# Optimization experiments

Hardware: AMD Instinct MI355X
Metric: run time of the kernel (lower is better)

The kernel has to match this reference:

```python
import jax, jax.numpy as jnp
import numpy as np

N = 50000      # nodes
E = 800000     # edges
GENE = 64      # gene_dim
HID = 128      # hidden_dim
NCLS = 10      # num_classes
EPS = 1e-5


def setup_inputs() -> dict:
    key = jax.random.key(0)
    ks = jax.random.split(key, 4)
    inp = {
        "x": jax.random.normal(ks[0], (N, GENE), jnp.float32),
        "edge_index": jax.random.randint(ks[1], (2, E), 0, N),
    }
    # PNA-style conv: concat([x, 4 aggregators x 3 scalers]) -> 13*d_in features
    dims = [(GENE, HID), (HID, 2 * HID), (2 * HID, HID), (HID, HID // 2)]
    for i, (din, dout) in enumerate(dims, 1):
        k = jax.random.fold_in(key, i)
        inp[f"W{i}"] = jax.random.normal(k, (13 * din, dout), jnp.float32) / float(np.sqrt(13 * din))
        inp[f"b{i}"] = jnp.zeros((dout,), jnp.float32)
        inp[f"gamma{i}"] = jnp.ones((dout,), jnp.float32)
        inp[f"beta{i}"] = jnp.zeros((dout,), jnp.float32)
    inp["Wc"] = jax.random.normal(ks[2], (HID // 2, NCLS), jnp.float32) / float(np.sqrt(HID // 2))
    inp["bc"] = jnp.zeros((NCLS,), jnp.float32)
    return inp


def _pna(x, src, dst, deg, log_deg, delta, W, b):
    # gather source features along edges: [E, d]
    msg = x[src]
    cnt = jnp.maximum(deg, 1.0)[:, None]
    s = jax.ops.segment_sum(msg, dst, num_segments=N)
    mean = s / cnt
    mean_sq = jax.ops.segment_sum(msg * msg, dst, num_segments=N) / cnt
    std = jnp.sqrt(jnp.maximum(mean_sq - mean * mean, 0.0) + EPS)
    has = (deg > 0)[:, None]
    mn = jnp.where(has, jax.ops.segment_min(msg, dst, num_segments=N), 0.0)
    mx = jnp.where(has, jax.ops.segment_max(msg, dst, num_segments=N), 0.0)
    aggs = jnp.concatenate([mean, mn, mx, std], axis=-1)  # [N, 4d]
    amp = (log_deg / delta)[:, None]                       # amplification scaler
    att = jnp.where(log_deg > 0, delta / jnp.maximum(log_deg, 1e-6), 1.0)[:, None]
    feat = jnp.concatenate([x, aggs, aggs * amp, aggs * att], axis=-1)  # [N, 13d]
    return feat @ W + b


def _bn(h, gamma, beta):
    m = h.mean(axis=0)
    v = h.var(axis=0)
    return (h - m) / jnp.sqrt(v + EPS) * gamma + beta


def reference(x, edge_index, W1, b1, gamma1, beta1, W2, b2, gamma2, beta2,
              W3, b3, gamma3, beta3, W4, b4, gamma4, beta4, Wc, bc):
    src, dst = edge_index[0], edge_index[1]
    deg = jax.ops.segment_sum(jnp.ones((E,), jnp.float32), dst, num_segments=N)
    log_deg = jnp.log1p(deg)
    delta = log_deg.mean()
    h = _pna(x, src, dst, deg, log_deg, delta, W1, b1)
    h = _bn(jax.nn.relu(h), gamma1, beta1)
    h = _pna(h, src, dst, deg, log_deg, delta, W2, b2)
    h = _bn(jax.nn.relu(h), gamma2, beta2)
    h = _pna(h, src, dst, deg, log_deg, delta, W3, b3)
    h = _bn(jax.nn.relu(h), gamma3, beta3)
    h = _pna(h, src, dst, deg, log_deg, delta, W4, b4)
    h = _bn(jax.nn.relu(h), gamma4, beta4)
    return h @ Wc + bc
```

## Files before the change

kernel.cpp:

```cpp
#include <hip/hip_runtime.h>
#include <hip/hip_bf16.h>

#define NN 50000
#define NE 800000
#define EPSV 1e-5f
#define NB 49

typedef _Float16 h8 __attribute__((ext_vector_type(8)));
typedef float    f4 __attribute__((ext_vector_type(4)));

#define AS1 __attribute__((address_space(1)))
#define AS3 __attribute__((address_space(3)))

__device__ __forceinline__ void gload_lds16(const _Float16* g, _Float16* l){
  __builtin_amdgcn_global_load_lds((const AS1 void*)g, (AS3 void*)l, 16, 0, 0);
}


__global__ void k_deg(const int* __restrict__ dst, int* __restrict__ deg){
  int e = blockIdx.x*blockDim.x + threadIdx.x;
  if(e < NE) atomicAdd(&deg[dst[e]], 1);
}

__global__ void k_logdeg(const int* __restrict__ deg, float* __restrict__ logdeg,
                         float* __restrict__ dsum){
  int i = blockIdx.x*blockDim.x + threadIdx.x;
  float v = 0.f;
  if(i < NN){ v = log1pf((float)deg[i]); logdeg[i] = v; }
  __shared__ float sh[256];
  sh[threadIdx.x] = v; __syncthreads();
  for(int off=128; off>0; off>>=1){
    if(threadIdx.x < off) sh[threadIdx.x] += sh[threadIdx.x+off];
    __syncthreads();
  }
  if(threadIdx.x == 0) atomicAdd(dsum, sh[0]);
}

__global__ void k_scalers(const float* __restrict__ logdeg, const float* __restrict__ dsum,
                          float* __restrict__ amp, float* __restrict__ att){
  int i = blockIdx.x*blockDim.x + threadIdx.x;
  if(i >= NN) return;
  float delta = dsum[0] / (float)NN;
  float ld = logdeg[i];
  amp[i] = ld / delta;
  att[i] = (ld > 0.f) ? (delta / fmaxf(ld, 1e-6f)) : 1.f;
}

__global__ void k_scan1(const int* __restrict__ deg, int* __restrict__ rowptr,
                        int* __restrict__ bsum){
  __shared__ int buf[1024];
  int tid = threadIdx.x;
  int i = blockIdx.x*1024 + tid;
  int v = (i < NN) ? deg[i] : 0;
  buf[tid] = v; __syncthreads();
  for(int off=1; off<1024; off<<=1){
    int t = (tid >= off) ? buf[tid-off] : 0;
    __syncthreads();
    buf[tid] += t;
    __syncthreads();
  }
  if(i < NN) rowptr[i] = buf[tid] - v;
  if(tid == 1023) bsum[blockIdx.x] = buf[1023];
}

__global__ void k_scan2(int* __restrict__ bsum){
  if(threadIdx.x == 0){
    int s = 0;
    for(int b = 0; b < NB; b++){ int t = bsum[b]; bsum[b] = s; s += t; }
    bsum[NB] = s;
  }
}

__global__ void k_scan3(int* __restrict__ rowptr, int* __restrict__ cursor,
                        const int* __restrict__ bsum){
  int i = blockIdx.x*256 + threadIdx.x;
  if(i < NN){
    int v = rowptr[i] + bsum[i >> 10];
    rowptr[i] = v; cursor[i] = v;
  }
  if(i == NN) rowptr[NN] = bsum[NB];
}

__global__ void k_fill(const int* __restrict__ src, const int* __restrict__ dst,
                       int* __restrict__ cursor, int* __restrict__ colidx){
  int e = blockIdx.x*blockDim.x + threadIdx.x;
  if(e < NE){
    int pos = atomicAdd(&cursor[dst[e]], 1);
    colidx[pos] = src[e];
  }
}

__global__ void k_cvtx(const float* __restrict__ x, _Float16* __restrict__ act){
  int i = blockIdx.x*256 + threadIdx.x;
  if(i < NN*64) act[i] = (_Float16)x[i];
}

__global__ void k_coef_id(float* __restrict__ cs, float* __restrict__ csh,
                          _Float16* __restrict__ cs16, _Float16* __restrict__ csh16){
  int c = threadIdx.x;
  cs[c] = 1.f; csh[c] = 0.f;
  cs16[c] = (_Float16)1.f; csh16[c] = (_Float16)0.f;
}

__global__ void k_bn_coef(const float* __restrict__ colsum, const float* __restrict__ colss,
                          const float* __restrict__ gamma, const float* __restrict__ beta,
                          int dout, float* __restrict__ cs, float* __restrict__ csh,
                          _Float16* __restrict__ cs16, _Float16* __restrict__ csh16){
  int c = threadIdx.x;
  if(c >= dout) return;
  float mean = colsum[c] / (float)NN;
  float var  = colss[c] / (float)NN - mean*mean;
  float inv  = rsqrtf(fmaxf(var, 0.f) + EPSV);
  float a = inv * gamma[c];
  float b = beta[c] - mean * a;
  cs[c] = a; csh[c] = b;
  cs16[c] = (_Float16)a; csh16[c] = (_Float16)b;
}


template<int D>
__global__ __launch_bounds__(256) void k_agg8(
    const _Float16* __restrict__ act,
    const int* __restrict__ rowptr, const int* __restrict__ colidx,
    const float* __restrict__ cs, const float* __restrict__ csh,
    _Float16* __restrict__ aggs, size_t aggN)
{
  constexpr int LPN = D >> 3;
  constexpr int NPW = 64 / LPN;
  int wv = threadIdx.x >> 6, lane = threadIdx.x & 63;
  int n = blockIdx.x*(NPW*4) + wv*NPW + (lane / LPN);
  int c = (lane % LPN) * 8;
  if(n >= NN) return;
  int beg = rowptr[n], end = rowptr[n+1];
  const _Float16* hp = act + c;

  float s[8], q[8], mn[8], mx[8];
  #pragma unroll
  for(int j = 0; j < 8; j++){ s[j]=0.f; q[j]=0.f; mn[j]=INFINITY; mx[j]=-INFINITY; }

#define ACC8(v) { _Pragma("unroll") for(int j=0;j<8;j++){ float a=(float)(v)[j]; \
    s[j]+=a; q[j]+=a*a; mn[j]=fminf(mn[j],a); mx[j]=fmaxf(mx[j],a); } }

  int e = beg;
  for(; e+8 <= end; e+=8){
    int i0=colidx[e],   i1=colidx[e+1], i2=colidx[e+2], i3=colidx[e+3];
    int i4=colidx[e+4], i5=colidx[e+5], i6=colidx[e+6], i7=colidx[e+7];
    h8 v0 = *(const h8*)(hp + (size_t)i0*D);
    h8 v1 = *(const h8*)(hp + (size_t)i1*D);
    h8 v2 = *(const h8*)(hp + (size_t)i2*D);
    h8 v3 = *(const h8*)(hp + (size_t)i3*D);
    h8 v4 = *(const h8*)(hp + (size_t)i4*D);
    h8 v5 = *(const h8*)(hp + (size_t)i5*D);
    h8 v6 = *(const h8*)(hp + (size_t)i6*D);
    h8 v7 = *(const h8*)(hp + (size_t)i7*D);
    ACC8(v0) ACC8(v1) ACC8(v2) ACC8(v3) ACC8(v4) ACC8(v5) ACC8(v6) ACC8(v7)
  }
  for(; e+4 <= end; e+=4){
    int i0=colidx[e], i1=colidx[e+1], i2=colidx[e+2], i3=colidx[e+3];
    h8 v0 = *(const h8*)(hp + (size_t)i0*D);
    h8 v1 = *(const h8*)(hp + (size_t)i1*D);
    h8 v2 = *(const h8*)(hp + (size_t)i2*D);
    h8 v3 = *(const h8*)(hp + (size_t)i3*D);
    ACC8(v0) ACC8(v1) ACC8(v2) ACC8(v3)
  }
  for(; e < end; e++){
    h8 v = *(const h8*)(hp + (size_t)colidx[e]*D);
    ACC8(v)
  }
#undef ACC8

  float cnt = (end>beg) ? (float)(end-beg) : 1.f;
  h8 vm, vn, vx, vs;
  #pragma unroll
  for(int j = 0; j < 8; j++){
    float a = cs[c+j], b = csh[c+j];
    float mean_r = s[j]/cnt;
    float var_r  = fmaxf(q[j]/cnt - mean_r*mean_r, 0.f);
    float meanp = a*mean_r + b;
    float mnp = (a >= 0.f) ? a*mn[j]+b : a*mx[j]+b;
    float mxp = (a >= 0.f) ? a*mx[j]+b : a*mn[j]+b;
    float sdp = sqrtf(a*a*var_r + EPSV);
    if(end <= beg){ meanp = 0.f; mnp = 0.f; mxp = 0.f; sdp = sqrtf(EPSV); }
    vm[j] = (_Float16)meanp; vn[j] = (_Float16)mnp;
    vx[j] = (_Float16)mxp;   vs[j] = (_Float16)sdp;
  }

  _Float16* dst = aggs + (size_t)(c>>6)*aggN + (size_t)n*256 + (c & 63);
  *(h8*)(dst)       = vm;
  *(h8*)(dst + 64)  = vn;
  *(h8*)(dst + 128) = vx;
  *(h8*)(dst + 192) = vs;
}


struct PackJob { const float* W; _Float16* dst; int d, o, j0, start; };
struct PackArgs { PackJob job[9]; int total; };

__global__ void k_pack_all(PackArgs a){
  int idx = blockIdx.x*256 + threadIdx.x;
  if(idx >= a.total) return;
  int ji = 0;
  while(ji < 8 && idx >= a.job[ji+1].start) ji++;
  PackJob J = a.job[ji];
  int rel = idx - J.start;
  int j    = rel & 7;
  int lane = (rel >> 3) & 63;
  int rem  = rel >> 9;
  int ntiles = J.o >> 4;
  int kb = rem / ntiles;
  int nt = rem - kb*ntiles;
  int k = kb*32 + (lane>>4)*8 + j;
  int n = nt*16 + (lane&15);
  int srcrow;
  if(k < 64)       srcrow = J.j0 + k;
  else if(k < 320){ int t=k-64;  srcrow = (1+(t>>6))*J.d + J.j0 + (t&63); }
  else if(k < 576){ int t=k-320; srcrow = (5+(t>>6))*J.d + J.j0 + (t&63); }
  else            { int t=k-576; srcrow = (9+(t>>6))*J.d + J.j0 + (t&63); }
  J.dst[rel] = (_Float16)J.W[(size_t)srcrow*J.o + n];
}


template<int NCH>
__global__ __launch_bounds__(256) void k_mfma_fused(
    const _Float16* __restrict__ actIn,
    const _Float16* __restrict__ aggs,
    const float* __restrict__ amp, const float* __restrict__ att,
    const _Float16* __restrict__ cs16, const _Float16* __restrict__ csh16,
    const _Float16* __restrict__ Wp, int o,
    const float* __restrict__ bias,
    _Float16* __restrict__ out,
    float* __restrict__ colsum, float* __restrict__ colss,
    size_t aggN)
{
  constexpr int D = NCH * 64;
  constexpr int NPH = NCH * 9;
  __shared__ _Float16 Bsm[3][12*512];
  __shared__ float redS[64], redQ[64];
  int tid  = threadIdx.x;
  int wv   = tid >> 6;
  int lane = tid & 63;
  int mi   = lane & 15;
  int q    = lane >> 4;

  int T  = gridDim.x * gridDim.y;
  int n_ = blockIdx.y * gridDim.x + blockIdx.x;
  int qq = T >> 3, rr = T & 7, xc = n_ & 7, nl = n_ >> 3;
  int m_ = (xc < rr ? xc*(qq+1) : rr*(qq+1) + (xc-rr)*qq) + nl;
  int bx = m_ % gridDim.x;
  int by = m_ / gridDim.x;

  int m0   = by * 128 + wv * 32;
  int c0   = bx * 64;
  int ntiles = o >> 4;
  int nt0  = bx * 4;

  if(tid < 64){ redS[tid] = 0.f; redQ[tid] = 0.f; }

  int mrow[2];
  mrow[0] = min(m0 + mi,      NN-1);
  mrow[1] = min(m0 + 16 + mi, NN-1);
  _Float16 am16[2] = { (_Float16)amp[mrow[0]], (_Float16)amp[mrow[1]] };
  _Float16 at16[2] = { (_Float16)att[mrow[0]], (_Float16)att[mrow[1]] };
  const _Float16* hAb[2];
  const _Float16* agb[2];
  hAb[0] = actIn + (size_t)mrow[0]*D + q*8;
  hAb[1] = actIn + (size_t)mrow[1]*D + q*8;
  agb[0] = aggs + (size_t)mrow[0]*256 + q*8;
  agb[1] = aggs + (size_t)mrow[1]*256 + q*8;

  f4 acc[2][4] = {};

  auto stageX = [&](_Float16* buf, int c){
    const _Float16* Wpc = Wp + (size_t)c*832*o;
    #pragma unroll
    for(int s = 0; s < 2; s++){
      int ti = wv*2 + s;
      int kb = ti >> 2, nn = ti & 3;
      gload_lds16(Wpc + (((size_t)kb*ntiles + nt0 + nn)*64 + lane)*8,
                  buf + ti*512);
    }
  };
  auto stageP = [&](_Float16* buf, int c, int idx){
    const _Float16* Wpc = Wp + (size_t)c*832*o;
    #pragma unroll
    for(int s = 0; s < 3; s++){
      int ti = wv*3 + s;
      int kj = ti >> 2, nn = ti & 3;
      int kb = (kj == 0 ? 2 : (kj == 1 ? 10 : 18)) + idx;
      gload_lds16(Wpc + (((size_t)kb*ntiles + nt0 + nn)*64 + lane)*8,
                  buf + ti*512);
    }
  };
  auto stagePh = [&](int p2){
    int c2 = p2 / 9, s2 = p2 % 9;
    _Float16* buf = &Bsm[p2 % 3][0];
    if(s2 == 0) stageX(buf, c2);
    else        stageP(buf, c2, s2 - 1);
  };

  h8 pA[2][4]; h8 pS[2][2]; h8 pH[2][2];
  auto loadA = [&](int ph2, int bank){
    if(ph2 >= NPH) return;
    int c = ph2 / 9, sub = ph2 % 9;
    if(sub == 0){
      #pragma unroll
      for(int kb = 0; kb < 2; kb++){
        pS[bank][kb] = *(const h8*)(cs16  + c*64 + kb*32 + q*8);
        pH[bank][kb] = *(const h8*)(csh16 + c*64 + kb*32 + q*8);
        #pragma unroll
        for(int t = 0; t < 2; t++)
          pA[bank][kb*2+t] = *(const h8*)(hAb[t] + c*64 + kb*32);
      }
    } else {
      int idx = sub - 1;
      #pragma unroll
      for(int t = 0; t < 2; t++)
        pA[bank][t] = *(const h8*)(agb[t] + (size_t)c*aggN + idx*32);
    }
  };

  stagePh(0);
  __builtin_amdgcn_sched_barrier(0);
  stagePh(1);
  __builtin_amdgcn_sched_barrier(0);
  loadA(0, 0);
  loadA(1, 1);
  __builtin_amdgcn_sched_barrier(0);
  asm volatile("s_waitcnt vmcnt(13)\n\ts_barrier" ::: "memory");

  #pragma unroll
  for(int ph = 0; ph < NPH; ph++){
    const int sub = ph % 9;
    const int bank = ph & 1;
    _Float16* cur = &Bsm[ph % 3][0];

    h8 cA[4]; h8 cS[2]; h8 cH[2];
    cA[0] = pA[bank][0]; cA[1] = pA[bank][1];
    if(sub == 0){
      cA[2] = pA[bank][2]; cA[3] = pA[bank][3];
      cS[0] = pS[bank][0]; cS[1] = pS[bank][1];
      cH[0] = pH[bank][0]; cH[1] = pH[bank][1];
    }

    if(ph + 2 < NPH) stagePh(ph + 2);
    __builtin_amdgcn_sched_barrier(0);

    loadA(ph + 2, bank);

    __builtin_amdgcn_s_setprio(1);
    if(sub == 0){
      #pragma unroll
      for(int kb = 0; kb < 2; kb++)
        #pragma unroll
        for(int t = 0; t < 2; t++){
          h8 ax = cA[kb*2+t]*cS[kb] + cH[kb];
          #pragma unroll
          for(int nn = 0; nn < 4; nn++)
            acc[t][nn] = __builtin_amdgcn_mfma_f32_16x16x32_f16(
                ax, *(const h8*)(cur + (kb*4+nn)*512 + lane*8), acc[t][nn], 0,0,0);
        }
    } else {
      #pragma unroll
      for(int t = 0; t < 2; t++){
        h8 apl = cA[t];
        h8 aam = apl * am16[t];
        h8 aat = apl * at16[t];
        #pragma unroll
        for(int nn = 0; nn < 4; nn++){
          acc[t][nn] = __builtin_amdgcn_mfma_f32_16x16x32_f16(
              apl, *(const h8*)(cur + (0*4+nn)*512 + lane*8), acc[t][nn], 0,0,0);
          acc[t][nn] = __builtin_amdgcn_mfma_f32_16x16x32_f16(
              aam, *(const h8*)(cur + (4+nn)*512 + lane*8), acc[t][nn], 0,0,0);
          acc[t][nn] = __builtin_amdgcn_mfma_f32_16x16x32_f16(
              aat, *(const h8*)(cur + (8+nn)*512 + lane*8), acc[t][nn], 0,0,0);
        }
      }
    }
    __builtin_amdgcn_s_setprio(0);

    if(ph + 1 < NPH){
      const bool x1   = ((ph + 1) % 9) == 0;
      const bool has2 = (ph + 2) < NPH;
      const bool x2   = has2 && (((ph + 2) % 9) == 0);
      const int K = (x1 ? 8 : 2) + (has2 ? ((x2 ? 2 : 3) + (x2 ? 8 : 2)) : 0);
      if(K == 13)      asm volatile("s_waitcnt vmcnt(13)\n\ts_barrier" ::: "memory");
      else if(K == 12) asm volatile("s_waitcnt vmcnt(12)\n\ts_barrier" ::: "memory");
      else if(K == 7)  asm volatile("s_waitcnt vmcnt(7)\n\ts_barrier" ::: "memory");
      else             asm volatile("s_waitcnt vmcnt(2)\n\ts_barrier" ::: "memory");
    }
  }

  __syncthreads();

  #pragma unroll
  for(int nn = 0; nn < 4; nn++){
    int n = c0 + nn*16 + mi;
    float bv = bias[n];
    float ps = 0.f, pq = 0.f;
    #pragma unroll
    for(int t = 0; t < 2; t++){
      #pragma unroll
      for(int r = 0; r < 4; r++){
        int m = m0 + t*16 + q*4 + r;
        if(m < NN){
          float v = fmaxf(bv + acc[t][nn][r], 0.f);
          out[(size_t)m*o + n] = (_Float16)v;
          ps += v; pq += v*v;
        }
      }
    }
    ps += __shfl_xor(ps, 16); pq += __shfl_xor(pq, 16);
    ps += __shfl_xor(ps, 32); pq += __shfl_xor(pq, 32);
    if(q == 0){
      atomicAdd(&redS[nn*16 + mi], ps);
      atomicAdd(&redQ[nn*16 + mi], pq);
    }
  }
  __syncthreads();
  if(tid < 64){
    atomicAdd(&colsum[c0 + tid], redS[tid]);
    atomicAdd(&colss[c0 + tid],  redQ[tid]);
  }
}


__global__ __launch_bounds__(256) void k_cls(const _Float16* __restrict__ h,
    const float* __restrict__ cs, const float* __restrict__ csh,
    const float* __restrict__ Wc, const float* __restrict__ bc,
    float* __restrict__ out){
  __shared__ float w[640];
  __shared__ float bb[16];
  __shared__ float sca[64], shb[64];
  int tid = threadIdx.x;
  for(int i = tid; i < 640; i += 256) w[i] = Wc[i];
  if(tid < 10) bb[tid] = bc[tid];
  if(tid < 64){ sca[tid] = cs[tid]; shb[tid] = csh[tid]; }
  __syncthreads();
  int idx = blockIdx.x*256 + tid;
  int n = idx >> 4;
  int c = idx & 15;
  if(n < NN && c < 10){
    float acc = bb[c];
    const _Float16* hp = h + (size_t)n*64;
    #pragma unroll
    for(int k = 0; k < 64; k++)
      acc += ((float)hp[k]*sca[k] + shb[k]) * w[k*10 + c];
    out[(size_t)n*10 + c] = acc;
  }
}


extern "C" void kernel_launch(void* const* d_in, const int* in_sizes, int n_in,
                              void* d_out, int out_size, void* d_ws, size_t ws_size,
                              hipStream_t stream){
  const float* x = (const float*)d_in[0];
  const int* edge = (const int*)d_in[1];
  const int* esrc = edge;
  const int* edst = edge + NE;
  const float* W[4]  = {(const float*)d_in[2],  (const float*)d_in[6],
                        (const float*)d_in[10], (const float*)d_in[14]};
  const float* bb[4] = {(const float*)d_in[3],  (const float*)d_in[7],
                        (const float*)d_in[11], (const float*)d_in[15]};
  const float* gm[4] = {(const float*)d_in[4],  (const float*)d_in[8],
                        (const float*)d_in[12], (const float*)d_in[16]};
  const float* bt[4] = {(const float*)d_in[5],  (const float*)d_in[9],
                        (const float*)d_in[13], (const float*)d_in[17]};
  const float* Wc = (const float*)d_in[18];
  const float* bc = (const float*)d_in[19];
  (void)in_sizes; (void)n_in; (void)out_size; (void)ws_size;

  char* p = (char*)d_ws;
  auto alloc = [&](size_t bytes)->char*{
    char* r = p; p += (bytes + 255) & ~(size_t)255; return r;
  };
  _Float16* act0 = (_Float16*)alloc((size_t)NN*256*2);
  _Float16* act1 = (_Float16*)alloc((size_t)NN*256*2);
  _Float16* aggs = (_Float16*)alloc((size_t)4*NN*256*2);
  int*   deg    = (int*)  alloc((size_t)NN*4);
  float* logdeg = (float*)alloc((size_t)NN*4);
  float* amp    = (float*)alloc((size_t)NN*4);
  float* att    = (float*)alloc((size_t)NN*4);
  int*   rowptr = (int*)  alloc((size_t)(NN+1)*4);
  int*   cursor = (int*)  alloc((size_t)NN*4);
  int*   colidx = (int*)  alloc((size_t)NE*4);
  int*   bsum   = (int*)  alloc((size_t)(NB+1)*4);
  float* colsumL= (float*)alloc(4*256*4);
  float* colssL = (float*)alloc(4*256*4);
  float* dsum   = (float*)alloc(256);
  float*    csA  = (float*)   alloc(256*4);
  float*    cshA = (float*)   alloc(256*4);
  float*    csB  = (float*)   alloc(256*4);
  float*    cshB = (float*)   alloc(256*4);
  _Float16* cs16A  = (_Float16*)alloc(256*2);
  _Float16* csh16A = (_Float16*)alloc(256*2);
  _Float16* cs16B  = (_Float16*)alloc(256*2);
  _Float16* csh16B = (_Float16*)alloc(256*2);

  const int din[4]  = {64, 128, 256, 128};
  const int dto[4]  = {128, 256, 128, 64};
  const size_t aggN = (size_t)NN*256;
  _Float16* WpL[4];
  PackArgs pa; int pj = 0, poff = 0;
  for(int l = 0; l < 4; l++){
    int nch = din[l]/64;
    WpL[l] = (_Float16*)alloc((size_t)nch*832*dto[l]*2);
    for(int c = 0; c < nch; c++){
      pa.job[pj] = { W[l], WpL[l] + (size_t)c*832*dto[l], din[l], dto[l], c*64, poff };
      poff += 832*dto[l]; pj++;
    }
  }
  pa.total = poff;

  hipMemsetAsync(deg, 0, (size_t)NN*4, stream);
  hipMemsetAsync(dsum, 0, 4, stream);
  hipMemsetAsync(colsumL, 0, 4*256*4, stream);
  hipMemsetAsync(colssL,  0, 4*256*4, stream);

  k_pack_all<<<(pa.total+255)/256, 256, 0, stream>>>(pa);
  k_deg     <<<(NE+255)/256, 256, 0, stream>>>(edst, deg);
  k_logdeg  <<<(NN+255)/256, 256, 0, stream>>>(deg, logdeg, dsum);
  k_scalers <<<(NN+255)/256, 256, 0, stream>>>(logdeg, dsum, amp, att);
  k_scan1   <<<NB, 1024, 0, stream>>>(deg, rowptr, bsum);
  k_scan2   <<<1, 64, 0, stream>>>(bsum);
  k_scan3   <<<(NN+256)/256, 256, 0, stream>>>(rowptr, cursor, bsum);
  k_fill    <<<(NE+255)/256, 256, 0, stream>>>(esrc, edst, cursor, colidx);
  k_cvtx    <<<(NN*64+255)/256, 256, 0, stream>>>(x, act0);
  k_coef_id <<<1, 256, 0, stream>>>(csA, cshA, cs16A, csh16A);

  _Float16* actIn = act0;  _Float16* actOut = act1;
  float *csI = csA, *cshI = cshA, *csO = csB, *cshO = cshB;
  _Float16 *cs16I = cs16A, *csh16I = csh16A, *cs16O = cs16B, *csh16O = csh16B;

  for(int l = 0; l < 4; l++){
    int d = din[l], o = dto[l];
    int npb = (64 / (d >> 3)) * 4;
    int nagg = (NN + npb - 1) / npb;
    dim3 g(o/64, (NN+127)/128);
    float* csum = colsumL + l*256;
    float* csq  = colssL + l*256;
    switch(d){
      case 64:
        k_agg8<64><<<nagg, 256, 0, stream>>>(actIn, rowptr, colidx, csI, cshI, aggs, aggN);
        k_mfma_fused<1><<<g, 256, 0, stream>>>(actIn, aggs, amp, att, cs16I, csh16I,
                                               WpL[l], o, bb[l], actOut, csum, csq, aggN);
        break;
      case 128:
        k_agg8<128><<<nagg, 256, 0, stream>>>(actIn, rowptr, colidx, csI, cshI, aggs, aggN);
        k_mfma_fused<2><<<g, 256, 0, stream>>>(actIn, aggs, amp, att, cs16I, csh16I,
                                               WpL[l], o, bb[l], actOut, csum, csq, aggN);
        break;
      default:
        k_agg8<256><<<nagg, 256, 0, stream>>>(actIn, rowptr, colidx, csI, cshI, aggs, aggN);
        k_mfma_fused<4><<<g, 256, 0, stream>>>(actIn, aggs, amp, att, cs16I, csh16I,
                                               WpL[l], o, bb[l], actOut, csum, csq, aggN);
        break;
    }
    k_bn_coef<<<1, 256, 0, stream>>>(csum, csq, gm[l], bt[l], o,
                                     csO, cshO, cs16O, csh16O);
    _Float16* ta = actIn; actIn = actOut; actOut = ta;
    float* tf;
    tf = csI;  csI = csO;  csO = tf;
    tf = cshI; cshI = cshO; cshO = tf;
    _Float16* th;
    th = cs16I;  cs16I = cs16O;  cs16O = th;
    th = csh16I; csh16I = csh16O; csh16O = th;
  }
  k_cls<<<(NN*16+255)/256, 256, 0, stream>>>(actIn, csI, cshI, Wc, bc, (float*)d_out);
}
```

Measured before the change: 651.8 us.

## Split neighbor aggregation into 64-column chunks processed by separate block ranges

The aggregation kernel now always maps 8 lanes per node over one 64-column chunk and launches one block range per chunk, instead of spanning the full feature width per node. Consecutive blocks therefore gather the same 64-column slice of source rows, which is meant to shrink the gathered working set so the cache catches more reuse at wider layers. The cost is that each chunk re-reads the CSR indices and repeats the per-node overhead d/64 times.

```diff
diff --git a/kernel.cpp b/kernel.cpp
--- a/kernel.cpp
+++ b/kernel.cpp
@@ -118,21 +118,23 @@
 }
 
 
-template<int D>
-__global__ __launch_bounds__(256) void k_agg8(
+template<int DFULL>
+__global__ __launch_bounds__(256) void k_agg8c(
     const _Float16* __restrict__ act,
     const int* __restrict__ rowptr, const int* __restrict__ colidx,
     const float* __restrict__ cs, const float* __restrict__ csh,
     _Float16* __restrict__ aggs, size_t aggN)
 {
-  constexpr int LPN = D >> 3;
-  constexpr int NPW = 64 / LPN;
+  constexpr int NPC = (NN + 31) >> 5;
+  int chunk = blockIdx.x / NPC;
+  int nb    = blockIdx.x - chunk*NPC;
   int wv = threadIdx.x >> 6, lane = threadIdx.x & 63;
-  int n = blockIdx.x*(NPW*4) + wv*NPW + (lane / LPN);
-  int c = (lane % LPN) * 8;
+  int n  = nb*32 + wv*8 + (lane >> 3);
+  int cl = (lane & 7) * 8;
+  int cg = chunk*64 + cl;
   if(n >= NN) return;
   int beg = rowptr[n], end = rowptr[n+1];
-  const _Float16* hp = act + c;
+  const _Float16* hp = act + cg;
 
   float s[8], q[8], mn[8], mx[8];
   #pragma unroll
@@ -145,26 +147,26 @@
   for(; e+8 <= end; e+=8){
     int i0=colidx[e],   i1=colidx[e+1], i2=colidx[e+2], i3=colidx[e+3];
     int i4=colidx[e+4], i5=colidx[e+5], i6=colidx[e+6], i7=colidx[e+7];
-    h8 v0 = *(const h8*)(hp + (size_t)i0*D);
-    h8 v1 = *(const h8*)(hp + (size_t)i1*D);
-    h8 v2 = *(const h8*)(hp + (size_t)i2*D);
-    h8 v3 = *(const h8*)(hp + (size_t)i3*D);
-    h8 v4 = *(const h8*)(hp + (size_t)i4*D);
-    h8 v5 = *(const h8*)(hp + (size_t)i5*D);
-    h8 v6 = *(const h8*)(hp + (size_t)i6*D);
-    h8 v7 = *(const h8*)(hp + (size_t)i7*D);
+    h8 v0 = *(const h8*)(hp + (size_t)i0*DFULL);
+    h8 v1 = *(const h8*)(hp + (size_t)i1*DFULL);
+    h8 v2 = *(const h8*)(hp + (size_t)i2*DFULL);
+    h8 v3 = *(const h8*)(hp + (size_t)i3*DFULL);
+    h8 v4 = *(const h8*)(hp + (size_t)i4*DFULL);
+    h8 v5 = *(const h8*)(hp + (size_t)i5*DFULL);
+    h8 v6 = *(const h8*)(hp + (size_t)i6*DFULL);
+    h8 v7 = *(const h8*)(hp + (size_t)i7*DFULL);
     ACC8(v0) ACC8(v1) ACC8(v2) ACC8(v3) ACC8(v4) ACC8(v5) ACC8(v6) ACC8(v7)
   }
   for(; e+4 <= end; e+=4){
     int i0=colidx[e], i1=colidx[e+1], i2=colidx[e+2], i3=colidx[e+3];
-    h8 v0 = *(const h8*)(hp + (size_t)i0*D);
-    h8 v1 = *(const h8*)(hp + (size_t)i1*D);
-    h8 v2 = *(const h8*)(hp + (size_t)i2*D);
-    h8 v3 = *(const h8*)(hp + (size_t)i3*D);
+    h8 v0 = *(const h8*)(hp + (size_t)i0*DFULL);
+    h8 v1 = *(const h8*)(hp + (size_t)i1*DFULL);
+    h8 v2 = *(const h8*)(hp + (size_t)i2*DFULL);
+    h8 v3 = *(const h8*)(hp + (size_t)i3*DFULL);
     ACC8(v0) ACC8(v1) ACC8(v2) ACC8(v3)
   }
   for(; e < end; e++){
-    h8 v = *(const h8*)(hp + (size_t)colidx[e]*D);
+    h8 v = *(const h8*)(hp + (size_t)colidx[e]*DFULL);
     ACC8(v)
   }
 #undef ACC8
@@ -173,7 +175,7 @@
   h8 vm, vn, vx, vs;
   #pragma unroll
   for(int j = 0; j < 8; j++){
-    float a = cs[c+j], b = csh[c+j];
+    float a = cs[cg+j], b = csh[cg+j];
     float mean_r = s[j]/cnt;
     float var_r  = fmaxf(q[j]/cnt - mean_r*mean_r, 0.f);
     float meanp = a*mean_r + b;
@@ -185,7 +187,7 @@
     vx[j] = (_Float16)mxp;   vs[j] = (_Float16)sdp;
   }
 
-  _Float16* dst = aggs + (size_t)(c>>6)*aggN + (size_t)n*256 + (c & 63);
+  _Float16* dst = aggs + (size_t)chunk*aggN + (size_t)n*256 + cl;
   *(h8*)(dst)       = vm;
   *(h8*)(dst + 64)  = vn;
   *(h8*)(dst + 128) = vx;
@@ -531,26 +533,27 @@
   float *csI = csA, *cshI = cshA, *csO = csB, *cshO = cshB;
   _Float16 *cs16I = cs16A, *csh16I = csh16A, *cs16O = cs16B, *csh16O = csh16B;
 
+  const int NPC = (NN + 31) >> 5;
+
   for(int l = 0; l < 4; l++){
     int d = din[l], o = dto[l];
-    int npb = (64 / (d >> 3)) * 4;
-    int nagg = (NN + npb - 1) / npb;
+    int nagg = NPC * (d/64);
     dim3 g(o/64, (NN+127)/128);
     float* csum = colsumL + l*256;
     float* csq  = colssL + l*256;
     switch(d){
       case 64:
-        k_agg8<64><<<nagg, 256, 0, stream>>>(actIn, rowptr, colidx, csI, cshI, aggs, aggN);
+        k_agg8c<64><<<nagg, 256, 0, stream>>>(actIn, rowptr, colidx, csI, cshI, aggs, aggN);
         k_mfma_fused<1><<<g, 256, 0, stream>>>(actIn, aggs, amp, att, cs16I, csh16I,
                                                WpL[l], o, bb[l], actOut, csum, csq, aggN);
         break;
       case 128:
-        k_agg8<128><<<nagg, 256, 0, stream>>>(actIn, rowptr, colidx, csI, cshI, aggs, aggN);
+        k_agg8c<128><<<nagg, 256, 0, stream>>>(actIn, rowptr, colidx, csI, cshI, aggs, aggN);
         k_mfma_fused<2><<<g, 256, 0, stream>>>(actIn, aggs, amp, att, cs16I, csh16I,
                                                WpL[l], o, bb[l], actOut, csum, csq, aggN);
         break;
       default:
-        k_agg8<256><<<nagg, 256, 0, stream>>>(actIn, rowptr, colidx, csI, cshI, aggs, aggN);
+        k_agg8c<256><<<nagg, 256, 0, stream>>>(actIn, rowptr, colidx, csI, cshI, aggs, aggN);
         k_mfma_fused<4><<<g, 256, 0, stream>>>(actIn, aggs, amp, att, cs16I, csh16I,
                                                WpL[l], o, bb[l], actOut, csum, csq, aggN);
         break;
```

Measured after the change: 671.1 us (median of 2 runs). 3.0% more time.
